# Optimization experiments

Hardware: AMD Instinct MI355X
Metric: run time of the kernel (lower is better)

## Reference

```python
import jax, jax.numpy as jnp
import numpy as np

B, T, C = 4, 2048, 1024
H = 16
D = C // H  # 64


def setup_inputs() -> dict:
    key = jax.random.key(0)
    ks = jax.random.split(key, 3)
    scale = 1.0 / np.sqrt(C)
    return {
        "x": jax.random.normal(ks[0], (B, T, C), dtype=jnp.float32),
        "W_attn": jax.random.normal(ks[1], (C, 3 * C), dtype=jnp.float32) * scale,
        "b_attn": jnp.zeros((3 * C,), dtype=jnp.float32),
        "W_proj": jax.random.normal(ks[2], (C, C), dtype=jnp.float32) * scale,
        "b_proj": jnp.zeros((C,), dtype=jnp.float32),
    }


def reference(x, W_attn, b_attn, W_proj, b_proj):
    b, t, c = x.shape
    qkv = x @ W_attn + b_attn                      # [B,T,3C]
    q, k, v = jnp.split(qkv, 3, axis=-1)           # each [B,T,C]
    to_heads = lambda z: z.reshape(b, t, H, D).transpose(0, 2, 1, 3)  # [B,H,T,D]
    q, k, v = to_heads(q), to_heads(k), to_heads(v)
    scores = jnp.einsum("bhtd,bhsd->bhts", q, k) / jnp.sqrt(jnp.float32(D))
    causal = jnp.tril(jnp.ones((t, t), dtype=bool))  # [T,T]
    scores = jnp.where(causal[None, None], scores, jnp.finfo(scores.dtype).min)
    attn = jax.nn.softmax(scores, axis=-1)           # [B,H,T,T]
    out = jnp.einsum("bhts,bhsd->bhtd", attn, v)     # [B,H,T,D]
    out = out.transpose(0, 2, 1, 3).reshape(b, t, c)
    return out @ W_proj + b_proj
```

## Files before the change

### kernel.cpp

```cpp
#include <hip/hip_runtime.h>
#include <hip/hip_bf16.h>

typedef __bf16 bf16_t;
typedef __attribute__((ext_vector_type(8))) __bf16 bf16x8;
typedef __attribute__((ext_vector_type(4))) float f32x4;
typedef __attribute__((ext_vector_type(4))) unsigned short u16x4;
typedef __attribute__((ext_vector_type(4))) unsigned int u32x4;

#define B_DIM 4
#define T_DIM 2048
#define C_DIM 1024
#define H_DIM 16
#define D_DIM 64
#define M_TOK (B_DIM * T_DIM)
#define N_QKV (3 * C_DIM)
#define NT    (T_DIM / 64)
#define KSTR  72
#define TILE_E (64 * KSTR)
#define CSC   0.18033688011112042f

__device__ __forceinline__ void gload_lds16(const bf16_t* g, bf16_t* l) {
  __builtin_amdgcn_global_load_lds((const __attribute__((address_space(1))) void*)(g),
                                   (__attribute__((address_space(3))) void*)(l), 16, 0, 0);
}

__global__ void cvt_f32_to_bf16(const float* __restrict__ in, bf16_t* __restrict__ out, int n4) {
  int i = blockIdx.x * blockDim.x + threadIdx.x;
  if (i >= n4) return;
  float4 v = ((const float4*)in)[i];
  struct alignas(8) bv4 { bf16_t x, y, z, w; };
  bv4 o;
  o.x = (bf16_t)v.x; o.y = (bf16_t)v.y; o.z = (bf16_t)v.z; o.w = (bf16_t)v.w;
  ((bv4*)out)[i] = o;
}

__global__ void transpose_f32_to_bf16(const float* __restrict__ in, bf16_t* __restrict__ out,
                                      int K, int N) {
  __shared__ float tile[32][33];
  int bx = blockIdx.x * 32;
  int by = blockIdx.y * 32;
  int tx = threadIdx.x, ty = threadIdx.y;
#pragma unroll
  for (int i = 0; i < 32; i += 8)
    tile[ty + i][tx] = in[(size_t)(by + ty + i) * N + bx + tx];
  __syncthreads();
#pragma unroll
  for (int i = 0; i < 32; i += 8)
    out[(size_t)(bx + ty + i) * K + by + tx] = (bf16_t)tile[tx][ty + i];
}

#define BM 128
#define BN 128
#define BK 32

__global__ __launch_bounds__(256, 4)
void gemm_bt_bias(const bf16_t* __restrict__ A, const bf16_t* __restrict__ Bt,
                  const float* __restrict__ bias, bf16_t* __restrict__ Cb,
                  int M, int N, int K) {
  __shared__ alignas(16) bf16_t As[BM * BK];
  __shared__ alignas(16) bf16_t Bs[BN * BK];
  const int tid = threadIdx.x;
  const int lane = tid & 63;
  const int wave = tid >> 6;
  const int wr = (wave >> 1) * 64, wc = (wave & 1) * 64;
  const int quad = lane >> 4, l16 = lane & 15;
  const int row0 = blockIdx.x * BM, col0 = blockIdx.y * BN;

  const int srow = wave * 32 + (lane >> 2);
  const int scol = (lane & 3) * 8;
  const bf16_t* Ag = A + (size_t)(row0 + srow) * K + scol;
  const bf16_t* Bg = Bt + (size_t)(col0 + srow) * K + scol;
  bf16_t* AsW = &As[(wave * 32) * BK];
  bf16_t* BsW = &Bs[(wave * 32) * BK];

  f32x4 acc[4][4];
#pragma unroll
  for (int i = 0; i < 4; ++i)
#pragma unroll
    for (int j = 0; j < 4; ++j)
      acc[i][j] = (f32x4){0.f, 0.f, 0.f, 0.f};

  for (int k0 = 0; k0 < K; k0 += BK) {
    __syncthreads();
    gload_lds16(Ag + k0, AsW);
    gload_lds16(Ag + k0 + (size_t)16 * K, AsW + 16 * BK);
    gload_lds16(Bg + k0, BsW);
    gload_lds16(Bg + k0 + (size_t)16 * K, BsW + 16 * BK);
    __syncthreads();
    bf16x8 af[4], bfr[4];
#pragma unroll
    for (int i = 0; i < 4; ++i)
      af[i] = *(const bf16x8*)&As[(wr + i * 16 + l16) * BK + quad * 8];
#pragma unroll
    for (int j = 0; j < 4; ++j)
      bfr[j] = *(const bf16x8*)&Bs[(wc + j * 16 + l16) * BK + quad * 8];
#pragma unroll
    for (int i = 0; i < 4; ++i)
#pragma unroll
      for (int j = 0; j < 4; ++j)
        acc[i][j] = __builtin_amdgcn_mfma_f32_16x16x32_bf16(af[i], bfr[j], acc[i][j], 0, 0, 0);
  }

#pragma unroll
  for (int i = 0; i < 4; ++i)
#pragma unroll
    for (int j = 0; j < 4; ++j) {
      int col = col0 + wc + j * 16 + l16;
      float bv = bias[col];
#pragma unroll
      for (int r = 0; r < 4; ++r) {
        int row = row0 + wr + i * 16 + quad * 4 + r;
        Cb[(size_t)row * N + col] = (bf16_t)(acc[i][j][r] + bv);
      }
    }
}

__global__ __launch_bounds__(256, 4)
void gemm_bt_bias_n64(const bf16_t* __restrict__ A, const bf16_t* __restrict__ Bt,
                      const float* __restrict__ bias, float* __restrict__ Cf,
                      int M, int N, int K) {
  __shared__ alignas(16) bf16_t As[BM * BK];
  __shared__ alignas(16) bf16_t Bs[64 * BK];
  const int tid = threadIdx.x;
  const int lane = tid & 63;
  const int wave = tid >> 6;
  const int wr = (wave >> 1) * 64, wc = (wave & 1) * 32;
  const int quad = lane >> 4, l16 = lane & 15;
  const int row0 = blockIdx.x * BM, col0 = blockIdx.y * 64;

  const int sr = lane >> 2;
  const int scol = (lane & 3) * 8;
  const bf16_t* Ag = A + (size_t)(row0 + wave * 32 + sr) * K + scol;
  const bf16_t* Bg = Bt + (size_t)(col0 + wave * 16 + sr) * K + scol;
  bf16_t* AsW = &As[(wave * 32) * BK];
  bf16_t* BsW = &Bs[(wave * 16) * BK];

  f32x4 acc[4][2];
#pragma unroll
  for (int i = 0; i < 4; ++i)
#pragma unroll
    for (int j = 0; j < 2; ++j)
      acc[i][j] = (f32x4){0.f, 0.f, 0.f, 0.f};

  for (int k0 = 0; k0 < K; k0 += BK) {
    __syncthreads();
    gload_lds16(Ag + k0, AsW);
    gload_lds16(Ag + k0 + (size_t)16 * K, AsW + 16 * BK);
    gload_lds16(Bg + k0, BsW);
    __syncthreads();
    bf16x8 af[4], bfr[2];
#pragma unroll
    for (int i = 0; i < 4; ++i)
      af[i] = *(const bf16x8*)&As[(wr + i * 16 + l16) * BK + quad * 8];
#pragma unroll
    for (int j = 0; j < 2; ++j)
      bfr[j] = *(const bf16x8*)&Bs[(wc + j * 16 + l16) * BK + quad * 8];
#pragma unroll
    for (int i = 0; i < 4; ++i)
#pragma unroll
      for (int j = 0; j < 2; ++j)
        acc[i][j] = __builtin_amdgcn_mfma_f32_16x16x32_bf16(af[i], bfr[j], acc[i][j], 0, 0, 0);
  }

#pragma unroll
  for (int i = 0; i < 4; ++i)
#pragma unroll
    for (int j = 0; j < 2; ++j) {
      int col = col0 + wc + j * 16 + l16;
      float bv = bias[col];
#pragma unroll
      for (int r = 0; r < 4; ++r) {
        int row = row0 + wr + i * 16 + quad * 4 + r;
        Cf[(size_t)row * N + col] = acc[i][j][r] + bv;
      }
    }
}

__global__ __launch_bounds__(256, 4)
void attn_fwd(const bf16_t* __restrict__ qkv, bf16_t* __restrict__ out) {
  __shared__ alignas(16) bf16_t Ks[2][TILE_E];
  __shared__ alignas(16) bf16_t Vt[2][TILE_E];

  const int tid = threadIdx.x;
  const int lane = tid & 63;
  const int wave = tid >> 6;
  const int quad = lane >> 4, l16 = lane & 15;
  const int qlo = blockIdx.x;
  const int qhi = NT - 1 - qlo;
  const int h = blockIdx.y, b = blockIdx.z;
  const size_t tokBase = (size_t)b * T_DIM;

  const bf16_t* qpl = qkv + (tokBase + qlo * 64 + wave * 16 + l16) * N_QKV + h * D_DIM;
  const bf16_t* qph = qkv + (tokBase + qhi * 64 + wave * 16 + l16) * N_QKV + h * D_DIM;
  bf16x8 ql0 = *(const bf16x8*)(qpl + quad * 8);
  bf16x8 ql1 = *(const bf16x8*)(qpl + 32 + quad * 8);
  bf16x8 qh0 = *(const bf16x8*)(qph + quad * 8);
  bf16x8 qh1 = *(const bf16x8*)(qph + 32 + quad * 8);

  f32x4 ol[4], oh[4];
#pragma unroll
  for (int dt = 0; dt < 4; ++dt) {
    ol[dt] = (f32x4){0.f, 0.f, 0.f, 0.f};
    oh[dt] = (f32x4){0.f, 0.f, 0.f, 0.f};
  }
  float ll = 0.f, lh = 0.f;

  const int tx = tid & 15, ty = tid >> 4;
  const int vswz = ((tx >> 2) & 3) * 8;
  const int vcol = (8 * (ty & 3) + 4 * ((ty >> 2) & 1) + 32 * (ty >> 3)) ^ vswz;
  const f32x4 zero4 = (f32x4){0.f, 0.f, 0.f, 0.f};

  u16x4 kreg[4], vreg[4];
  const bf16_t* kb0 = qkv + (tokBase + ty * 4) * N_QKV + h * D_DIM + C_DIM + tx * 4;
#pragma unroll
  for (int r = 0; r < 4; ++r) kreg[r] = *(const u16x4*)(kb0 + (size_t)r * N_QKV);
#pragma unroll
  for (int r = 0; r < 4; ++r) vreg[r] = *(const u16x4*)(kb0 + (size_t)r * N_QKV + C_DIM);
#pragma unroll
  for (int r = 0; r < 4; ++r)
    *(u16x4*)&Ks[0][(ty * 4 + r) * KSTR + tx * 4] = kreg[r];
#pragma unroll
  for (int i = 0; i < 4; ++i) {
    u16x4 p = (u16x4){vreg[0][i], vreg[1][i], vreg[2][i], vreg[3][i]};
    *(u16x4*)&Vt[0][(tx * 4 + i) * KSTR + vcol] = p;
  }
  __syncthreads();

  for (int t = 0; t <= qhi; ++t) {
    const int cur = t & 1;
    const bool lo = (t <= qlo);

    if (t < qhi) {
      const bf16_t* kb = qkv + (tokBase + (t + 1) * 64 + ty * 4) * N_QKV + h * D_DIM + C_DIM + tx * 4;
#pragma unroll
      for (int r = 0; r < 4; ++r) kreg[r] = *(const u16x4*)(kb + (size_t)r * N_QKV);
#pragma unroll
      for (int r = 0; r < 4; ++r) vreg[r] = *(const u16x4*)(kb + (size_t)r * N_QKV + C_DIM);
    }

    f32x4 svl[4], svh[4];
    __builtin_amdgcn_s_setprio(1);
#pragma unroll
    for (int ct = 0; ct < 4; ++ct) {
      bf16x8 kf0 = *(const bf16x8*)&Ks[cur][(ct * 16 + l16) * KSTR + quad * 8];
      bf16x8 kf1 = *(const bf16x8*)&Ks[cur][(ct * 16 + l16) * KSTR + 32 + quad * 8];
      if (lo) {
        svl[ct] = __builtin_amdgcn_mfma_f32_16x16x32_bf16(kf0, ql0, zero4, 0, 0, 0);
        svl[ct] = __builtin_amdgcn_mfma_f32_16x16x32_bf16(kf1, ql1, svl[ct], 0, 0, 0);
      }
      svh[ct] = __builtin_amdgcn_mfma_f32_16x16x32_bf16(kf0, qh0, zero4, 0, 0, 0);
      svh[ct] = __builtin_amdgcn_mfma_f32_16x16x32_bf16(kf1, qh1, svh[ct], 0, 0, 0);
    }
    __builtin_amdgcn_s_setprio(0);
    if (t == qlo) {
      const int qr = wave * 16 + l16;
#pragma unroll
      for (int ct = 0; ct < 4; ++ct)
#pragma unroll
        for (int r = 0; r < 4; ++r)
          if (ct * 16 + quad * 4 + r > qr) svl[ct][r] = -INFINITY;
    }
    if (t == qhi) {
      const int qr = wave * 16 + l16;
#pragma unroll
      for (int ct = 0; ct < 4; ++ct)
#pragma unroll
        for (int r = 0; r < 4; ++r)
          if (ct * 16 + quad * 4 + r > qr) svh[ct][r] = -INFINITY;
    }

    struct alignas(4) bpair { bf16_t lo, hi; };
    bf16x8 pl0, pl1, ph0, ph1;
    if (lo) {
      float rsum = 0.f;
      unsigned int lw[8];
#pragma unroll
      for (int ct = 0; ct < 4; ++ct) {
        float e0 = __builtin_amdgcn_exp2f(svl[ct][0] * CSC);
        float e1 = __builtin_amdgcn_exp2f(svl[ct][1] * CSC);
        float e2 = __builtin_amdgcn_exp2f(svl[ct][2] * CSC);
        float e3 = __builtin_amdgcn_exp2f(svl[ct][3] * CSC);
        rsum += (e0 + e1) + (e2 + e3);
        bpair w0 = {(bf16_t)e0, (bf16_t)e1};
        bpair w1 = {(bf16_t)e2, (bf16_t)e3};
        lw[ct * 2 + 0] = __builtin_bit_cast(unsigned int, w0);
        lw[ct * 2 + 1] = __builtin_bit_cast(unsigned int, w1);
      }
      rsum += __shfl_xor(rsum, 16);
      rsum += __shfl_xor(rsum, 32);
      ll += rsum;
      u32x4 pw0 = (u32x4){lw[0], lw[1], lw[2], lw[3]};
      u32x4 pw1 = (u32x4){lw[4], lw[5], lw[6], lw[7]};
      pl0 = __builtin_bit_cast(bf16x8, pw0);
      pl1 = __builtin_bit_cast(bf16x8, pw1);
    }
    {
      float rsum = 0.f;
      unsigned int lw[8];
#pragma unroll
      for (int ct = 0; ct < 4; ++ct) {
        float e0 = __builtin_amdgcn_exp2f(svh[ct][0] * CSC);
        float e1 = __builtin_amdgcn_exp2f(svh[ct][1] * CSC);
        float e2 = __builtin_amdgcn_exp2f(svh[ct][2] * CSC);
        float e3 = __builtin_amdgcn_exp2f(svh[ct][3] * CSC);
        rsum += (e0 + e1) + (e2 + e3);
        bpair w0 = {(bf16_t)e0, (bf16_t)e1};
        bpair w1 = {(bf16_t)e2, (bf16_t)e3};
        lw[ct * 2 + 0] = __builtin_bit_cast(unsigned int, w0);
        lw[ct * 2 + 1] = __builtin_bit_cast(unsigned int, w1);
      }
      rsum += __shfl_xor(rsum, 16);
      rsum += __shfl_xor(rsum, 32);
      lh += rsum;
      u32x4 pw0 = (u32x4){lw[0], lw[1], lw[2], lw[3]};
      u32x4 pw1 = (u32x4){lw[4], lw[5], lw[6], lw[7]};
      ph0 = __builtin_bit_cast(bf16x8, pw0);
      ph1 = __builtin_bit_cast(bf16x8, pw1);
    }

    if (t < qhi) {
#pragma unroll
      for (int r = 0; r < 4; ++r)
        *(u16x4*)&Ks[cur ^ 1][(ty * 4 + r) * KSTR + tx * 4] = kreg[r];
#pragma unroll
      for (int i = 0; i < 4; ++i) {
        u16x4 p = (u16x4){vreg[0][i], vreg[1][i], vreg[2][i], vreg[3][i]};
        *(u16x4*)&Vt[cur ^ 1][(tx * 4 + i) * KSTR + vcol] = p;
      }
    }

    __builtin_amdgcn_s_setprio(1);
#pragma unroll
    for (int dt = 0; dt < 4; ++dt) {
      const int vc = (quad * 8) ^ (dt * 8);
      bf16x8 vf0 = *(const bf16x8*)&Vt[cur][(dt * 16 + l16) * KSTR + vc];
      bf16x8 vf1 = *(const bf16x8*)&Vt[cur][(dt * 16 + l16) * KSTR + 32 + vc];
      if (lo) {
        ol[dt] = __builtin_amdgcn_mfma_f32_16x16x32_bf16(vf0, pl0, ol[dt], 0, 0, 0);
        ol[dt] = __builtin_amdgcn_mfma_f32_16x16x32_bf16(vf1, pl1, ol[dt], 0, 0, 0);
      }
      oh[dt] = __builtin_amdgcn_mfma_f32_16x16x32_bf16(vf0, ph0, oh[dt], 0, 0, 0);
      oh[dt] = __builtin_amdgcn_mfma_f32_16x16x32_bf16(vf1, ph1, oh[dt], 0, 0, 0);
    }
    __builtin_amdgcn_s_setprio(0);

    __syncthreads();
  }

  struct alignas(8) bh4 { bf16_t a, b, c, d; };
  {
    float rl = 1.0f / ll;
    bf16_t* op = out + (tokBase + qlo * 64 + wave * 16 + l16) * C_DIM + h * D_DIM;
#pragma unroll
    for (int dt = 0; dt < 4; ++dt) {
      bh4 v = {(bf16_t)(ol[dt][0] * rl), (bf16_t)(ol[dt][1] * rl),
               (bf16_t)(ol[dt][2] * rl), (bf16_t)(ol[dt][3] * rl)};
      *(bh4*)(op + dt * 16 + quad * 4) = v;
    }
  }
  {
    float rl = 1.0f / lh;
    bf16_t* op = out + (tokBase + qhi * 64 + wave * 16 + l16) * C_DIM + h * D_DIM;
#pragma unroll
    for (int dt = 0; dt < 4; ++dt) {
      bh4 v = {(bf16_t)(oh[dt][0] * rl), (bf16_t)(oh[dt][1] * rl),
               (bf16_t)(oh[dt][2] * rl), (bf16_t)(oh[dt][3] * rl)};
      *(bh4*)(op + dt * 16 + quad * 4) = v;
    }
  }
}

extern "C" void kernel_launch(void* const* d_in, const int* in_sizes, int n_in,
                              void* d_out, int out_size, void* d_ws, size_t ws_size,
                              hipStream_t stream) {
  const float* x      = (const float*)d_in[0];
  const float* W_attn = (const float*)d_in[1];
  const float* b_attn = (const float*)d_in[2];
  const float* W_proj = (const float*)d_in[3];
  const float* b_proj = (const float*)d_in[4];
  float* out = (float*)d_out;

  char* ws = (char*)d_ws;
  bf16_t* xb   = (bf16_t*)ws;  ws += (size_t)M_TOK * C_DIM * 2;
  bf16_t* Wat  = (bf16_t*)ws;  ws += (size_t)N_QKV * C_DIM * 2;
  bf16_t* Wpt  = (bf16_t*)ws;  ws += (size_t)C_DIM * C_DIM * 2;
  bf16_t* qkv  = (bf16_t*)ws;  ws += (size_t)M_TOK * N_QKV * 2;
  bf16_t* attn = (bf16_t*)ws;  ws += (size_t)M_TOK * C_DIM * 2;

  {
    int n4 = (M_TOK * C_DIM) / 4;
    cvt_f32_to_bf16<<<n4 / 256, 256, 0, stream>>>(x, xb, n4);
  }
  transpose_f32_to_bf16<<<dim3(N_QKV / 32, C_DIM / 32), dim3(32, 8), 0, stream>>>(W_attn, Wat, C_DIM, N_QKV);
  transpose_f32_to_bf16<<<dim3(C_DIM / 32, C_DIM / 32), dim3(32, 8), 0, stream>>>(W_proj, Wpt, C_DIM, C_DIM);

  gemm_bt_bias<<<dim3(M_TOK / BM, N_QKV / BN), 256, 0, stream>>>(
      xb, Wat, b_attn, qkv, M_TOK, N_QKV, C_DIM);

  attn_fwd<<<dim3(NT / 2, H_DIM, B_DIM), 256, 0, stream>>>(qkv, attn);

  gemm_bt_bias_n64<<<dim3(M_TOK / BM, C_DIM / 64), 256, 0, stream>>>(
      attn, Wpt, b_proj, out, M_TOK, C_DIM, C_DIM);
}
```

Baseline: 272.4 us.

## Replace both GEMMs with a triple-buffered 256x128 tile kernel using swizzled LDS

Replaces the two single-buffered 128x128 and 128x64 GEMM kernels with one templated 512-thread kernel. It uses 256x128 tiles, BK=64, three LDS stages filled by async global-to-LDS loads, and explicit vmcnt waits so loads overlap the MFMA work. An XOR swizzle on the LDS rows targets bank conflicts, and setprio raises priority around the MFMA block. In exchange it uses much more LDS (about 144KB per block), which lowers occupancy. The projection GEMM also gets fewer blocks.

```diff
diff --git a/kernel.cpp b/kernel.cpp
--- a/kernel.cpp
+++ b/kernel.cpp
@@ -49,29 +49,40 @@
     out[(size_t)(bx + ty + i) * K + by + tx] = (bf16_t)tile[tx][ty + i];
 }
 
-#define BM 128
-#define BN 128
-#define BK 32
-
-__global__ __launch_bounds__(256, 4)
-void gemm_bt_bias(const bf16_t* __restrict__ A, const bf16_t* __restrict__ Bt,
-                  const float* __restrict__ bias, bf16_t* __restrict__ Cb,
-                  int M, int N, int K) {
-  __shared__ alignas(16) bf16_t As[BM * BK];
-  __shared__ alignas(16) bf16_t Bs[BN * BK];
+template <typename OutT>
+__global__ __launch_bounds__(512, 2)
+void gemm256(const bf16_t* __restrict__ A, const bf16_t* __restrict__ Bt,
+             const float* __restrict__ bias, OutT* __restrict__ C,
+             int M, int N, int K) {
+  __shared__ alignas(16) bf16_t As[3][256 * 64];
+  __shared__ alignas(16) bf16_t Bs[3][128 * 64];
+
   const int tid = threadIdx.x;
   const int lane = tid & 63;
-  const int wave = tid >> 6;
-  const int wr = (wave >> 1) * 64, wc = (wave & 1) * 64;
+  const int w = tid >> 6;
+  const int w8 = w * 8;
   const int quad = lane >> 4, l16 = lane & 15;
-  const int row0 = blockIdx.x * BM, col0 = blockIdx.y * BN;
-
-  const int srow = wave * 32 + (lane >> 2);
-  const int scol = (lane & 3) * 8;
-  const bf16_t* Ag = A + (size_t)(row0 + srow) * K + scol;
-  const bf16_t* Bg = Bt + (size_t)(col0 + srow) * K + scol;
-  bf16_t* AsW = &As[(wave * 32) * BK];
-  bf16_t* BsW = &Bs[(wave * 32) * BK];
+  const int wrow = (w >> 1) * 64;
+  const int wcol = (w & 1) * 64;
+  const int row0 = blockIdx.x * 256, col0 = blockIdx.y * 128;
+
+  const int lrow = lane >> 3;
+  const int sw = ((lane & 7) ^ (lrow & 7)) * 8;
+  const bf16_t* Ag = A + (size_t)(row0 + w8 + lrow) * K + sw;
+  const bf16_t* Bg = Bt + (size_t)(col0 + w8 + lrow) * K + sw;
+
+  const int NTK = K >> 6;
+
+#define STAGE_TILE(tt, bi)                                                     \
+  do {                                                                         \
+    const size_t ko = (size_t)(tt) * 64;                                       \
+    _Pragma("unroll")                                                          \
+    for (int c = 0; c < 4; ++c)                                                \
+      gload_lds16(Ag + ko + (size_t)(c * 64) * K, &As[bi][(c * 64 + w8) * 64]);\
+    _Pragma("unroll")                                                          \
+    for (int c = 0; c < 2; ++c)                                                \
+      gload_lds16(Bg + ko + (size_t)(c * 64) * K, &Bs[bi][(c * 64 + w8) * 64]);\
+  } while (0)
 
   f32x4 acc[4][4];
 #pragma unroll
@@ -80,98 +91,57 @@
     for (int j = 0; j < 4; ++j)
       acc[i][j] = (f32x4){0.f, 0.f, 0.f, 0.f};
 
-  for (int k0 = 0; k0 < K; k0 += BK) {
-    __syncthreads();
-    gload_lds16(Ag + k0, AsW);
-    gload_lds16(Ag + k0 + (size_t)16 * K, AsW + 16 * BK);
-    gload_lds16(Bg + k0, BsW);
-    gload_lds16(Bg + k0 + (size_t)16 * K, BsW + 16 * BK);
-    __syncthreads();
-    bf16x8 af[4], bfr[4];
-#pragma unroll
-    for (int i = 0; i < 4; ++i)
-      af[i] = *(const bf16x8*)&As[(wr + i * 16 + l16) * BK + quad * 8];
-#pragma unroll
-    for (int j = 0; j < 4; ++j)
-      bfr[j] = *(const bf16x8*)&Bs[(wc + j * 16 + l16) * BK + quad * 8];
-#pragma unroll
-    for (int i = 0; i < 4; ++i)
+  STAGE_TILE(0, 0);
+  if (1 < NTK) STAGE_TILE(1, 1);
+
+  for (int t = 0; t < NTK; ++t) {
+    const int cur = t % 3;
+    asm volatile("s_barrier" ::: "memory");
+    if (t + 2 < NTK) {
+      STAGE_TILE(t + 2, (t + 2) % 3);
+      __builtin_amdgcn_sched_barrier(0);
+      asm volatile("s_waitcnt vmcnt(12)" ::: "memory");
+    } else if (t + 1 < NTK) {
+      asm volatile("s_waitcnt vmcnt(6)" ::: "memory");
+    } else {
+      asm volatile("s_waitcnt vmcnt(0)" ::: "memory");
+    }
+    __builtin_amdgcn_sched_barrier(0);
+    asm volatile("s_barrier" ::: "memory");
+
+    const bf16_t* AsT = &As[cur][0];
+    const bf16_t* BsT = &Bs[cur][0];
+#pragma unroll
+    for (int kk = 0; kk < 2; ++kk) {
+      bf16x8 af[4], bfr[4];
+      const int sl = (kk * 4 + quad) ^ (l16 & 7);
+#pragma unroll
+      for (int i = 0; i < 4; ++i)
+        af[i] = *(const bf16x8*)&AsT[(wrow + i * 16 + l16) * 64 + sl * 8];
 #pragma unroll
       for (int j = 0; j < 4; ++j)
-        acc[i][j] = __builtin_amdgcn_mfma_f32_16x16x32_bf16(af[i], bfr[j], acc[i][j], 0, 0, 0);
-  }
+        bfr[j] = *(const bf16x8*)&BsT[(wcol + j * 16 + l16) * 64 + sl * 8];
+      __builtin_amdgcn_s_setprio(1);
+#pragma unroll
+      for (int i = 0; i < 4; ++i)
+#pragma unroll
+        for (int j = 0; j < 4; ++j)
+          acc[i][j] = __builtin_amdgcn_mfma_f32_16x16x32_bf16(af[i], bfr[j], acc[i][j], 0, 0, 0);
+      __builtin_amdgcn_s_setprio(0);
+    }
+  }
+#undef STAGE_TILE
 
 #pragma unroll
   for (int i = 0; i < 4; ++i)
 #pragma unroll
     for (int j = 0; j < 4; ++j) {
-      int col = col0 + wc + j * 16 + l16;
+      int col = col0 + wcol + j * 16 + l16;
       float bv = bias[col];
 #pragma unroll
       for (int r = 0; r < 4; ++r) {
-        int row = row0 + wr + i * 16 + quad * 4 + r;
-        Cb[(size_t)row * N + col] = (bf16_t)(acc[i][j][r] + bv);
-      }
-    }
-}
-
-__global__ __launch_bounds__(256, 4)
-void gemm_bt_bias_n64(const bf16_t* __restrict__ A, const bf16_t* __restrict__ Bt,
-                      const float* __restrict__ bias, float* __restrict__ Cf,
-                      int M, int N, int K) {
-  __shared__ alignas(16) bf16_t As[BM * BK];
-  __shared__ alignas(16) bf16_t Bs[64 * BK];
-  const int tid = threadIdx.x;
-  const int lane = tid & 63;
-  const int wave = tid >> 6;
-  const int wr = (wave >> 1) * 64, wc = (wave & 1) * 32;
-  const int quad = lane >> 4, l16 = lane & 15;
-  const int row0 = blockIdx.x * BM, col0 = blockIdx.y * 64;
-
-  const int sr = lane >> 2;
-  const int scol = (lane & 3) * 8;
-  const bf16_t* Ag = A + (size_t)(row0 + wave * 32 + sr) * K + scol;
-  const bf16_t* Bg = Bt + (size_t)(col0 + wave * 16 + sr) * K + scol;
-  bf16_t* AsW = &As[(wave * 32) * BK];
-  bf16_t* BsW = &Bs[(wave * 16) * BK];
-
-  f32x4 acc[4][2];
-#pragma unroll
-  for (int i = 0; i < 4; ++i)
-#pragma unroll
-    for (int j = 0; j < 2; ++j)
-      acc[i][j] = (f32x4){0.f, 0.f, 0.f, 0.f};
-
-  for (int k0 = 0; k0 < K; k0 += BK) {
-    __syncthreads();
-    gload_lds16(Ag + k0, AsW);
-    gload_lds16(Ag + k0 + (size_t)16 * K, AsW + 16 * BK);
-    gload_lds16(Bg + k0, BsW);
-    __syncthreads();
-    bf16x8 af[4], bfr[2];
-#pragma unroll
-    for (int i = 0; i < 4; ++i)
-      af[i] = *(const bf16x8*)&As[(wr + i * 16 + l16) * BK + quad * 8];
-#pragma unroll
-    for (int j = 0; j < 2; ++j)
-      bfr[j] = *(const bf16x8*)&Bs[(wc + j * 16 + l16) * BK + quad * 8];
-#pragma unroll
-    for (int i = 0; i < 4; ++i)
-#pragma unroll
-      for (int j = 0; j < 2; ++j)
-        acc[i][j] = __builtin_amdgcn_mfma_f32_16x16x32_bf16(af[i], bfr[j], acc[i][j], 0, 0, 0);
-  }
-
-#pragma unroll
-  for (int i = 0; i < 4; ++i)
-#pragma unroll
-    for (int j = 0; j < 2; ++j) {
-      int col = col0 + wc + j * 16 + l16;
-      float bv = bias[col];
-#pragma unroll
-      for (int r = 0; r < 4; ++r) {
-        int row = row0 + wr + i * 16 + quad * 4 + r;
-        Cf[(size_t)row * N + col] = acc[i][j][r] + bv;
+        int row = row0 + wrow + i * 16 + quad * 4 + r;
+        C[(size_t)row * N + col] = (OutT)(acc[i][j][r] + bv);
       }
     }
 }
@@ -394,11 +364,11 @@
   transpose_f32_to_bf16<<<dim3(N_QKV / 32, C_DIM / 32), dim3(32, 8), 0, stream>>>(W_attn, Wat, C_DIM, N_QKV);
   transpose_f32_to_bf16<<<dim3(C_DIM / 32, C_DIM / 32), dim3(32, 8), 0, stream>>>(W_proj, Wpt, C_DIM, C_DIM);
 
-  gemm_bt_bias<<<dim3(M_TOK / BM, N_QKV / BN), 256, 0, stream>>>(
+  gemm256<bf16_t><<<dim3(M_TOK / 256, N_QKV / 128), 512, 0, stream>>>(
       xb, Wat, b_attn, qkv, M_TOK, N_QKV, C_DIM);
 
   attn_fwd<<<dim3(NT / 2, H_DIM, B_DIM), 256, 0, stream>>>(qkv, attn);
 
-  gemm_bt_bias_n64<<<dim3(M_TOK / BM, C_DIM / 64), 256, 0, stream>>>(
+  gemm256<float><<<dim3(M_TOK / 256, C_DIM / 128), 512, 0, stream>>>(
       attn, Wpt, b_proj, out, M_TOK, C_DIM, C_DIM);
 }
```

New measurement: 283.5 us. 4.1% more time.
